# Performance work log

Measured on AMD Instinct MI355X. Metric: run time of the kernel, lower is better.

The kernel has to match this reference:

```python
import jax, jax.numpy as jnp
import numpy as np

D_BLADE = 256
D_FFN = 1024
N_TOK = 8192
LN_EPS = 1e-5


def _derive_cayley_table():
    basis_gens = [(), (1,), (2,), (3,), (1, 2), (1, 3), (2, 3), (1, 2, 3)]
    gens_to_idx = {g: i for i, g in enumerate(basis_gens)}

    def reduce(a, b):
        gens = list(a) + list(b)
        sign = 1
        changed = True
        while changed:
            changed = False
            i = 0
            while i < len(gens) - 1:
                if gens[i] == gens[i + 1]:
                    gens.pop(i); gens.pop(i)
                    changed = True
                    if i > 0:
                        i -= 1
                elif gens[i] > gens[i + 1]:
                    gens[i], gens[i + 1] = gens[i + 1], gens[i]
                    sign *= -1
                    changed = True
                    i += 1
                else:
                    i += 1
        return gens_to_idx[tuple(gens)], sign

    return [[reduce(basis_gens[i], basis_gens[j]) for j in range(8)] for i in range(8)]


def _sparse_cayley():
    table = _derive_cayley_table()
    si, sj, tk, sg = [], [], [], []
    for i in range(8):
        for j in range(8):
            k, s = table[i][j]
            si.append(i); sj.append(j); tk.append(k); sg.append(float(s))
    return (np.array(si, np.int64), np.array(sj, np.int64),
            np.array(tk, np.int64), np.array(sg, np.float32))


def setup_inputs() -> dict:
    key = jax.random.key(0)
    ks = jax.random.split(key, 6)
    si, sj, tk, sg = _sparse_cayley()
    inv_d = 1.0 / np.sqrt(D_BLADE)
    inv_f = 1.0 / np.sqrt(D_FFN)
    return {
        "x": jax.random.normal(ks[0], (N_TOK, 8, D_BLADE), jnp.float32),
        "iw": jnp.full((64,), 0.1, jnp.float32),
        "sg": jnp.asarray(sg),
        "gg": jnp.asarray(0.5, jnp.float32),
        "gate_w": jax.random.normal(ks[1], (D_FFN, D_BLADE), jnp.float32) * inv_d,
        "up_w": jax.random.normal(ks[2], (D_FFN, D_BLADE), jnp.float32) * inv_d,
        "down_w": jax.random.normal(ks[3], (D_BLADE, D_FFN), jnp.float32) * inv_f,
        "ln_w": jnp.ones((D_BLADE,), jnp.float32),
        "ln_b": jnp.zeros((D_BLADE,), jnp.float32),
        "si": jnp.asarray(si),
        "sj": jnp.asarray(sj),
        "tk": jnp.asarray(tk),
    }


def reference(x, iw, sg, gg, gate_w, up_w, down_w, ln_w, ln_b, si, sj, tk):
    # x: (N, 8, D). 64 Cayley pairs: gather blades i,j, multiply, scatter-add to k.
    w = jax.nn.sigmoid(iw)                                  # (64,)
    products = x[:, si, :] * x[:, sj, :] * (sg * w)[None, :, None]  # (N,64,D)
    geo = jnp.zeros_like(x).at[:, tk, :].add(products)      # (N,8,D)
    g = jax.nn.sigmoid(gg)
    mixed = g * geo + (1.0 - g) * x
    # LayerNorm over last dim
    mu = jnp.mean(mixed, axis=-1, keepdims=True)
    var = jnp.mean(jnp.square(mixed - mu), axis=-1, keepdims=True)
    normed = (mixed - mu) * jax.lax.rsqrt(var + LN_EPS) * ln_w + ln_b
    # SwiGLU FFN
    h = jax.nn.silu(jnp.einsum("nbd,fd->nbf", normed, gate_w)) \
        * jnp.einsum("nbd,fd->nbf", normed, up_w)
    out = jnp.einsum("nbf,df->nbd", h, down_w)
    return x + out
```

## Files before the change

kernel.cpp:

```cpp
#include <hip/hip_runtime.h>
#include <hip/hip_bf16.h>

#define D_BLADE 256
#define D_FFN 1024
#define N_TOK 8192
#define M_TOTAL (N_TOK * 8)

typedef __attribute__((ext_vector_type(8))) short bf16x8;
typedef __attribute__((ext_vector_type(4))) float f32x4;
typedef __attribute__((address_space(1))) void gvoid;
typedef __attribute__((address_space(3))) void svoid;

__device__ __forceinline__ float sigm(float v) { return 1.0f / (1.0f + __expf(-v)); }

__global__ __launch_bounds__(256) void wconv_kernel(const float* __restrict__ g,
                                                    const float* __restrict__ u,
                                                    const float* __restrict__ dn,
                                                    __hip_bfloat16* __restrict__ wgu,
                                                    __hip_bfloat16* __restrict__ dwb) {
    int i = blockIdx.x * 256 + threadIdx.x;
    int f = i >> 8, k = i & 255;
    int t = f >> 4, fi = f & 15;
    wgu[(size_t)(t * 32 + fi) * 256 + k]      = __float2bfloat16(g[i]);
    wgu[(size_t)(t * 32 + 16 + fi) * 256 + k] = __float2bfloat16(u[i]);
    dwb[i] = __float2bfloat16(dn[i]);
}

__global__ __launch_bounds__(256) void geo_ln_kernel(
    const float* __restrict__ x, const float* __restrict__ iw,
    const float* __restrict__ sg, const float* __restrict__ gg,
    const float* __restrict__ lnw, const float* __restrict__ lnb,
    __hip_bfloat16* __restrict__ nrm)
{
    static constexpr int CK[64] = {
        0,1,2,3,4,5,6,7,
        1,0,4,5,2,3,7,6,
        2,4,0,6,1,7,3,5,
        3,5,6,0,7,1,2,4,
        4,2,1,7,0,6,5,3,
        5,3,7,1,6,0,4,2,
        6,7,3,2,5,4,0,1,
        7,6,5,4,3,2,1,0};
    __shared__ float coefs[64];
    __shared__ float redA[4][8];
    __shared__ float redB[4][8];
    const int tid = threadIdx.x;
    const int n = blockIdx.x;
    if (tid < 64) coefs[tid] = sg[tid] * sigm(iw[tid]);
    __syncthreads();

    const float* xp = x + (size_t)n * (8 * D_BLADE) + tid;
    float xa[8];
#pragma unroll
    for (int b = 0; b < 8; ++b) xa[b] = xp[b * D_BLADE];

    float geo[8] = {0.f,0.f,0.f,0.f,0.f,0.f,0.f,0.f};
#pragma unroll
    for (int p = 0; p < 64; ++p)
        geo[CK[p]] += coefs[p] * xa[p >> 3] * xa[p & 7];

    const float g = sigm(gg[0]);
    float mixed[8], sm[8], sq[8];
#pragma unroll
    for (int b = 0; b < 8; ++b) {
        mixed[b] = g * geo[b] + (1.0f - g) * xa[b];
        sm[b] = mixed[b];
        sq[b] = mixed[b] * mixed[b];
    }
#pragma unroll
    for (int off = 32; off > 0; off >>= 1) {
#pragma unroll
        for (int b = 0; b < 8; ++b) {
            sm[b] += __shfl_xor(sm[b], off, 64);
            sq[b] += __shfl_xor(sq[b], off, 64);
        }
    }
    const int wv = tid >> 6;
    if ((tid & 63) == 0) {
#pragma unroll
        for (int b = 0; b < 8; ++b) { redA[wv][b] = sm[b]; redB[wv][b] = sq[b]; }
    }
    __syncthreads();

    const float lw = lnw[tid], lb = lnb[tid];
    __hip_bfloat16* op = nrm + ((size_t)n * 8) * D_BLADE + tid;
#pragma unroll
    for (int b = 0; b < 8; ++b) {
        float ts = redA[0][b] + redA[1][b] + redA[2][b] + redA[3][b];
        float tq = redB[0][b] + redB[1][b] + redB[2][b] + redB[3][b];
        float mu = ts * (1.0f / 256.0f);
        float var = tq * (1.0f / 256.0f) - mu * mu;
        float rs = rsqrtf(var + 1e-5f);
        op[b * D_BLADE] = __float2bfloat16((mixed[b] - mu) * rs * lw + lb);
    }
}


#define STAGE(dst, srcbase, rowstride, kofs, NLOADS)                                 \
    _Pragma("unroll")                                                                 \
    for (int i = 0; i < (NLOADS); ++i) {                                              \
        int L = i * 4096 + tid * 16;                                                  \
        int r = L >> 7;                                                               \
        int Xs = (L & 127) ^ ((r & 7) << 4);                                          \
        const __hip_bfloat16* sp = (srcbase) + (size_t)(r) * (rowstride) + (kofs) + (Xs >> 1); \
        __builtin_amdgcn_global_load_lds((gvoid*)sp, (svoid*)((dst) + L), 16, 0, 0);  \
    }

__global__ __launch_bounds__(256, 4) void gu_kernel(
    const __hip_bfloat16* __restrict__ nrm,
    const __hip_bfloat16* __restrict__ wgu,
    __hip_bfloat16* __restrict__ h,
    int mbase)
{
    __shared__ char lds[32768];
    char* sA = lds;
    char* sB = lds + 16384;

    const int tid = threadIdx.x;
    const int l = tid & 63;
    const int w = tid >> 6;
    const int wm = w >> 1, wn = w & 1;
    const int rr = l & 15;
    const int kq = l >> 4;
    const int rsw = (rr & 7) << 4;

    const int cpx = gridDim.x >> 3;
    const int swz = (blockIdx.x & 7) * cpx + (blockIdx.x >> 3);
    const int bm = swz >> 4;
    const int n0 = (swz & 15) * 128;
    const int m0 = mbase + bm * 128;
    const int hr0 = bm * 128;
    const __hip_bfloat16* An = nrm + (size_t)m0 * D_BLADE;
    const __hip_bfloat16* Bn = wgu + (size_t)n0 * D_BLADE;

    const f32x4 zero = {0.f, 0.f, 0.f, 0.f};
    f32x4 acc[4][4];
#pragma unroll
    for (int mt = 0; mt < 4; ++mt)
#pragma unroll
        for (int nt = 0; nt < 4; ++nt) acc[mt][nt] = zero;

    STAGE(sA, An, D_BLADE, 0, 4)
    STAGE(sB, Bn, D_BLADE, 0, 4)
    asm volatile("s_waitcnt vmcnt(0)" ::: "memory");
    __builtin_amdgcn_sched_barrier(0);
    __syncthreads();

    for (int c = 0; c < 4; ++c) {
#pragma unroll
        for (int kk = 0; kk < 2; ++kk) {
            const int cb = (kk * 64 + kq * 16) ^ rsw;
            bf16x8 a[4], b[4];
#pragma unroll
            for (int nt = 0; nt < 4; ++nt)
                b[nt] = *reinterpret_cast<const bf16x8*>(sB + (wn * 64 + nt * 16 + rr) * 128 + cb);
#pragma unroll
            for (int mt = 0; mt < 4; ++mt)
                a[mt] = *reinterpret_cast<const bf16x8*>(sA + (wm * 64 + mt * 16 + rr) * 128 + cb);
            __builtin_amdgcn_s_setprio(1);
#pragma unroll
            for (int mt = 0; mt < 4; ++mt)
#pragma unroll
                for (int nt = 0; nt < 4; ++nt)
                    acc[mt][nt] = __builtin_amdgcn_mfma_f32_16x16x32_bf16(a[mt], b[nt], acc[mt][nt], 0, 0, 0);
            __builtin_amdgcn_s_setprio(0);
        }
        __syncthreads();
        if (c < 3) {
            STAGE(sA, An, D_BLADE, (c + 1) * 64, 4)
            STAGE(sB, Bn, D_BLADE, (c + 1) * 64, 4)
            asm volatile("s_waitcnt vmcnt(0)" ::: "memory");
            __builtin_amdgcn_sched_barrier(0);
            __syncthreads();
        }
    }

#pragma unroll
    for (int mt = 0; mt < 4; ++mt)
#pragma unroll
        for (int ntp = 0; ntp < 2; ++ntp) {
            f32x4 gv = acc[mt][2 * ntp];
            f32x4 uv = acc[mt][2 * ntp + 1];
            const int fcol = ((n0 + wn * 64) >> 1) + ntp * 16 + rr;
#pragma unroll
            for (int r = 0; r < 4; ++r) {
                int row = hr0 + wm * 64 + mt * 16 + kq * 4 + r;
                float ge = gv[r];
                float hv = ge * sigm(ge) * uv[r];
                h[(size_t)row * D_FFN + fcol] = __float2bfloat16(hv);
            }
        }
}

__global__ __launch_bounds__(256, 2) void down_kernel(
    const __hip_bfloat16* __restrict__ h,
    const __hip_bfloat16* __restrict__ dwb,
    const float* __restrict__ x,
    float* __restrict__ out,
    int mbase)
{
    __shared__ char lds[49152];
    char* sA = lds;
    char* sB = lds + 16384;

    const int tid = threadIdx.x;
    const int l = tid & 63;
    const int w = tid >> 6;
    const int wm = w >> 1, wn = w & 1;
    const int rr = l & 15;
    const int kq = l >> 4;
    const int rsw = (rr & 7) << 4;
    const int bm = blockIdx.x;
    const int hr0 = bm * 128;
    const __hip_bfloat16* An = h + (size_t)hr0 * D_FFN;
    const __hip_bfloat16* Bn = dwb;

    const f32x4 zero = {0.f, 0.f, 0.f, 0.f};
    f32x4 acc[4][8];
#pragma unroll
    for (int mt = 0; mt < 4; ++mt)
#pragma unroll
        for (int nt = 0; nt < 8; ++nt) acc[mt][nt] = zero;

    STAGE(sA, An, D_FFN, 0, 4)
    STAGE(sB, Bn, D_FFN, 0, 8)
    asm volatile("s_waitcnt vmcnt(0)" ::: "memory");
    __builtin_amdgcn_sched_barrier(0);
    __syncthreads();

    for (int c = 0; c < 16; ++c) {
#pragma unroll
        for (int kk = 0; kk < 2; ++kk) {
            const int cb = (kk * 64 + kq * 16) ^ rsw;
            bf16x8 a[4], b[8];
#pragma unroll
            for (int nt = 0; nt < 8; ++nt)
                b[nt] = *reinterpret_cast<const bf16x8*>(sB + (wn * 128 + nt * 16 + rr) * 128 + cb);
#pragma unroll
            for (int mt = 0; mt < 4; ++mt)
                a[mt] = *reinterpret_cast<const bf16x8*>(sA + (wm * 64 + mt * 16 + rr) * 128 + cb);
            __builtin_amdgcn_s_setprio(1);
#pragma unroll
            for (int mt = 0; mt < 4; ++mt)
#pragma unroll
                for (int nt = 0; nt < 8; ++nt)
                    acc[mt][nt] = __builtin_amdgcn_mfma_f32_16x16x32_bf16(a[mt], b[nt], acc[mt][nt], 0, 0, 0);
            __builtin_amdgcn_s_setprio(0);
        }
        __syncthreads();
        if (c < 15) {
            STAGE(sA, An, D_FFN, (c + 1) * 64, 4)
            STAGE(sB, Bn, D_FFN, (c + 1) * 64, 8)
            asm volatile("s_waitcnt vmcnt(0)" ::: "memory");
            __builtin_amdgcn_sched_barrier(0);
            __syncthreads();
        }
    }

#pragma unroll
    for (int mt = 0; mt < 4; ++mt)
#pragma unroll
        for (int nt = 0; nt < 8; ++nt)
#pragma unroll
            for (int r = 0; r < 4; ++r) {
                int gm = mbase + hr0 + wm * 64 + mt * 16 + kq * 4 + r;
                int d = wn * 128 + nt * 16 + rr;
                size_t idx = (size_t)gm * D_BLADE + d;
                out[idx] = x[idx] + acc[mt][nt][r];
            }
}

extern "C" void kernel_launch(void* const* d_in, const int* in_sizes, int n_in,
                              void* d_out, int out_size, void* d_ws, size_t ws_size,
                              hipStream_t stream) {
    const float* x   = (const float*)d_in[0];
    const float* iw  = (const float*)d_in[1];
    const float* sg  = (const float*)d_in[2];
    const float* gg  = (const float*)d_in[3];
    const float* gwf = (const float*)d_in[4];
    const float* uwf = (const float*)d_in[5];
    const float* dwf = (const float*)d_in[6];
    const float* lnw = (const float*)d_in[7];
    const float* lnb = (const float*)d_in[8];
    float* out = (float*)d_out;

    char* ws = (char*)d_ws;
    __hip_bfloat16* nrm = (__hip_bfloat16*)ws;
    size_t off = (size_t)M_TOTAL * D_BLADE * 2;
    __hip_bfloat16* wgu = (__hip_bfloat16*)(ws + off);
    off += (size_t)2 * D_FFN * D_BLADE * 2;
    __hip_bfloat16* dwb = (__hip_bfloat16*)(ws + off);
    off += (size_t)D_FFN * D_BLADE * 2;
    __hip_bfloat16* h = (__hip_bfloat16*)(ws + off);

    int S = 1;
    while (S < 64 && off + ((size_t)M_TOTAL / S) * D_FFN * 2 > ws_size) S <<= 1;
    const int MS = M_TOTAL / S;

    wconv_kernel<<<dim3((D_FFN * D_BLADE) / 256), dim3(256), 0, stream>>>(gwf, uwf, dwf, wgu, dwb);
    geo_ln_kernel<<<dim3(N_TOK), dim3(256), 0, stream>>>(x, iw, sg, gg, lnw, lnb, nrm);
    for (int s = 0; s < S; ++s) {
        gu_kernel<<<dim3((MS / 128) * 16), dim3(256), 0, stream>>>(nrm, wgu, h, s * MS);
        down_kernel<<<dim3(MS / 128), dim3(256), 0, stream>>>(h, dwb, x, out, s * MS);
    }
}
```

Measured before the change: 196.6 us.

## Map one token per wave in geo-LN, shrink down-GEMM M tile, split into two chunks

The geo/LayerNorm kernel now assigns one token per wavefront with float4 loads and packed bf16 stores. This removes the cross-wave shared-memory reduction and its block barrier. The down-projection kernel halves its M tile to 64 rows and raises the occupancy target to 4 blocks per CU, giving more blocks and less LDS per block at the cost of reloading the weight tile more often. The token range is also forced into at least two chunks, so the h buffer is smaller, possibly cache-resident, but more kernel launches run serially.

```diff
diff --git a/kernel.cpp b/kernel.cpp
--- a/kernel.cpp
+++ b/kernel.cpp
@@ -7,6 +7,7 @@
 #define M_TOTAL (N_TOK * 8)
 
 typedef __attribute__((ext_vector_type(8))) short bf16x8;
+typedef __attribute__((ext_vector_type(4))) short short4_t;
 typedef __attribute__((ext_vector_type(4))) float f32x4;
 typedef __attribute__((address_space(1))) void gvoid;
 typedef __attribute__((address_space(3))) void svoid;
@@ -42,30 +43,46 @@
         6,7,3,2,5,4,0,1,
         7,6,5,4,3,2,1,0};
     __shared__ float coefs[64];
-    __shared__ float redA[4][8];
-    __shared__ float redB[4][8];
     const int tid = threadIdx.x;
-    const int n = blockIdx.x;
+    const int lane = tid & 63;
+    const int wv = tid >> 6;
+    const int n = blockIdx.x * 4 + wv;
     if (tid < 64) coefs[tid] = sg[tid] * sigm(iw[tid]);
     __syncthreads();
 
-    const float* xp = x + (size_t)n * (8 * D_BLADE) + tid;
-    float xa[8];
-#pragma unroll
-    for (int b = 0; b < 8; ++b) xa[b] = xp[b * D_BLADE];
-
-    float geo[8] = {0.f,0.f,0.f,0.f,0.f,0.f,0.f,0.f};
-#pragma unroll
-    for (int p = 0; p < 64; ++p)
-        geo[CK[p]] += coefs[p] * xa[p >> 3] * xa[p & 7];
+    const float4* xp = reinterpret_cast<const float4*>(x + (size_t)n * (8 * D_BLADE)) + lane;
+    float4 xa[8];
+#pragma unroll
+    for (int b = 0; b < 8; ++b) xa[b] = xp[b * 64];
+
+    float geo[8][4] = {};
+#pragma unroll
+    for (int p = 0; p < 64; ++p) {
+        const float cf = coefs[p];
+        const float4 ai = xa[p >> 3];
+        const float4 aj = xa[p & 7];
+        geo[CK[p]][0] += cf * ai.x * aj.x;
+        geo[CK[p]][1] += cf * ai.y * aj.y;
+        geo[CK[p]][2] += cf * ai.z * aj.z;
+        geo[CK[p]][3] += cf * ai.w * aj.w;
+    }
 
     const float g = sigm(gg[0]);
-    float mixed[8], sm[8], sq[8];
+    float mixed[8][4];
+    float sm[8], sq[8];
 #pragma unroll
     for (int b = 0; b < 8; ++b) {
-        mixed[b] = g * geo[b] + (1.0f - g) * xa[b];
-        sm[b] = mixed[b];
-        sq[b] = mixed[b] * mixed[b];
+        const float xe[4] = {xa[b].x, xa[b].y, xa[b].z, xa[b].w};
+        float s = 0.f, q = 0.f;
+#pragma unroll
+        for (int e = 0; e < 4; ++e) {
+            float m = g * geo[b][e] + (1.0f - g) * xe[e];
+            mixed[b][e] = m;
+            s += m;
+            q += m * m;
+        }
+        sm[b] = s;
+        sq[b] = q;
     }
 #pragma unroll
     for (int off = 32; off > 0; off >>= 1) {
@@ -75,23 +92,23 @@
             sq[b] += __shfl_xor(sq[b], off, 64);
         }
     }
-    const int wv = tid >> 6;
-    if ((tid & 63) == 0) {
-#pragma unroll
-        for (int b = 0; b < 8; ++b) { redA[wv][b] = sm[b]; redB[wv][b] = sq[b]; }
-    }
-    __syncthreads();
-
-    const float lw = lnw[tid], lb = lnb[tid];
-    __hip_bfloat16* op = nrm + ((size_t)n * 8) * D_BLADE + tid;
+
+    const float4 lw4 = reinterpret_cast<const float4*>(lnw)[lane];
+    const float4 lb4 = reinterpret_cast<const float4*>(lnb)[lane];
+    const float lwe[4] = {lw4.x, lw4.y, lw4.z, lw4.w};
+    const float lbe[4] = {lb4.x, lb4.y, lb4.z, lb4.w};
 #pragma unroll
     for (int b = 0; b < 8; ++b) {
-        float ts = redA[0][b] + redA[1][b] + redA[2][b] + redA[3][b];
-        float tq = redB[0][b] + redB[1][b] + redB[2][b] + redB[3][b];
-        float mu = ts * (1.0f / 256.0f);
-        float var = tq * (1.0f / 256.0f) - mu * mu;
-        float rs = rsqrtf(var + 1e-5f);
-        op[b * D_BLADE] = __float2bfloat16((mixed[b] - mu) * rs * lw + lb);
+        const float mu = sm[b] * (1.0f / 256.0f);
+        const float var = sq[b] * (1.0f / 256.0f) - mu * mu;
+        const float rs = rsqrtf(var + 1e-5f);
+        short4_t o;
+#pragma unroll
+        for (int e = 0; e < 4; ++e) {
+            __hip_bfloat16 v = __float2bfloat16((mixed[b][e] - mu) * rs * lwe[e] + lbe[e]);
+            o[e] = *reinterpret_cast<short*>(&v);
+        }
+        *reinterpret_cast<short4_t*>(nrm + (size_t)n * (8 * D_BLADE) + b * D_BLADE + lane * 4) = o;
     }
 }
 
@@ -192,16 +209,16 @@
         }
 }
 
-__global__ __launch_bounds__(256, 2) void down_kernel(
+__global__ __launch_bounds__(256, 4) void down_kernel(
     const __hip_bfloat16* __restrict__ h,
     const __hip_bfloat16* __restrict__ dwb,
     const float* __restrict__ x,
     float* __restrict__ out,
     int mbase)
 {
-    __shared__ char lds[49152];
+    __shared__ char lds[40960];
     char* sA = lds;
-    char* sB = lds + 16384;
+    char* sB = lds + 8192;
 
     const int tid = threadIdx.x;
     const int l = tid & 63;
@@ -211,18 +228,18 @@
     const int kq = l >> 4;
     const int rsw = (rr & 7) << 4;
     const int bm = blockIdx.x;
-    const int hr0 = bm * 128;
+    const int hr0 = bm * 64;
     const __hip_bfloat16* An = h + (size_t)hr0 * D_FFN;
     const __hip_bfloat16* Bn = dwb;
 
     const f32x4 zero = {0.f, 0.f, 0.f, 0.f};
-    f32x4 acc[4][8];
-#pragma unroll
-    for (int mt = 0; mt < 4; ++mt)
+    f32x4 acc[2][8];
+#pragma unroll
+    for (int mt = 0; mt < 2; ++mt)
 #pragma unroll
         for (int nt = 0; nt < 8; ++nt) acc[mt][nt] = zero;
 
-    STAGE(sA, An, D_FFN, 0, 4)
+    STAGE(sA, An, D_FFN, 0, 2)
     STAGE(sB, Bn, D_FFN, 0, 8)
     asm volatile("s_waitcnt vmcnt(0)" ::: "memory");
     __builtin_amdgcn_sched_barrier(0);
@@ -232,16 +249,16 @@
 #pragma unroll
         for (int kk = 0; kk < 2; ++kk) {
             const int cb = (kk * 64 + kq * 16) ^ rsw;
-            bf16x8 a[4], b[8];
+            bf16x8 a[2], b[8];
 #pragma unroll
             for (int nt = 0; nt < 8; ++nt)
                 b[nt] = *reinterpret_cast<const bf16x8*>(sB + (wn * 128 + nt * 16 + rr) * 128 + cb);
 #pragma unroll
-            for (int mt = 0; mt < 4; ++mt)
-                a[mt] = *reinterpret_cast<const bf16x8*>(sA + (wm * 64 + mt * 16 + rr) * 128 + cb);
+            for (int mt = 0; mt < 2; ++mt)
+                a[mt] = *reinterpret_cast<const bf16x8*>(sA + (wm * 32 + mt * 16 + rr) * 128 + cb);
             __builtin_amdgcn_s_setprio(1);
 #pragma unroll
-            for (int mt = 0; mt < 4; ++mt)
+            for (int mt = 0; mt < 2; ++mt)
 #pragma unroll
                 for (int nt = 0; nt < 8; ++nt)
                     acc[mt][nt] = __builtin_amdgcn_mfma_f32_16x16x32_bf16(a[mt], b[nt], acc[mt][nt], 0, 0, 0);
@@ -249,7 +266,7 @@
         }
         __syncthreads();
         if (c < 15) {
-            STAGE(sA, An, D_FFN, (c + 1) * 64, 4)
+            STAGE(sA, An, D_FFN, (c + 1) * 64, 2)
             STAGE(sB, Bn, D_FFN, (c + 1) * 64, 8)
             asm volatile("s_waitcnt vmcnt(0)" ::: "memory");
             __builtin_amdgcn_sched_barrier(0);
@@ -258,12 +275,12 @@
     }
 
 #pragma unroll
-    for (int mt = 0; mt < 4; ++mt)
+    for (int mt = 0; mt < 2; ++mt)
 #pragma unroll
         for (int nt = 0; nt < 8; ++nt)
 #pragma unroll
             for (int r = 0; r < 4; ++r) {
-                int gm = mbase + hr0 + wm * 64 + mt * 16 + kq * 4 + r;
+                int gm = mbase + hr0 + wm * 32 + mt * 16 + kq * 4 + r;
                 int d = wn * 128 + nt * 16 + rr;
                 size_t idx = (size_t)gm * D_BLADE + d;
                 out[idx] = x[idx] + acc[mt][nt][r];
@@ -293,14 +310,14 @@
     off += (size_t)D_FFN * D_BLADE * 2;
     __hip_bfloat16* h = (__hip_bfloat16*)(ws + off);
 
-    int S = 1;
+    int S = 2;
     while (S < 64 && off + ((size_t)M_TOTAL / S) * D_FFN * 2 > ws_size) S <<= 1;
     const int MS = M_TOTAL / S;
 
     wconv_kernel<<<dim3((D_FFN * D_BLADE) / 256), dim3(256), 0, stream>>>(gwf, uwf, dwf, wgu, dwb);
-    geo_ln_kernel<<<dim3(N_TOK), dim3(256), 0, stream>>>(x, iw, sg, gg, lnw, lnb, nrm);
+    geo_ln_kernel<<<dim3(N_TOK / 4), dim3(256), 0, stream>>>(x, iw, sg, gg, lnw, lnb, nrm);
     for (int s = 0; s < S; ++s) {
         gu_kernel<<<dim3((MS / 128) * 16), dim3(256), 0, stream>>>(nrm, wgu, h, s * MS);
-        down_kernel<<<dim3(MS / 128), dim3(256), 0, stream>>>(h, dwb, x, out, s * MS);
-    }
-}
+        down_kernel<<<dim3(MS / 64), dim3(256), 0, stream>>>(h, dwb, x, out, s * MS);
+    }
+}
```

New measurement: 224.4 us. 1.14x slower.
